# Kernel tuning notes

Hardware: AMD Instinct MI355X
Metric: run time of the kernel (lower is better)

Reference implementation:

```python
import jax, jax.numpy as jnp
import numpy as np
import math

S, B, H, NH = 2048, 2, 2048, 16
HN = H // NH  # 128, head dim


def _rope_cache(seq_len, hn):
    # inv_freqs over even indices, half_hn entries
    inv_freqs = 0.0001 ** (jnp.arange(0, hn, 2, dtype=jnp.float32) / hn)
    pos = jnp.arange(seq_len, dtype=jnp.float32)
    angles = pos[:, None] * inv_freqs  # [s, hn/2]
    return jnp.cos(angles), jnp.sin(angles)


def _apply_rope(x, cos, sin):
    # x: [s, b, np, hn]; cos/sin: [s, hn/2] broadcast over b, np
    half = x.shape[-1] // 2
    c = cos[:, None, None, :]
    s = sin[:, None, None, :]
    left, right = x[..., :half], x[..., half:]
    return jnp.concatenate((c * left - s * right, s * left + c * right), axis=-1)


def setup_inputs() -> dict:
    key = jax.random.key(0)
    k0, k1, k2 = jax.random.split(key, 3)
    hidden_states = jax.random.normal(k0, (S, B, H), dtype=jnp.float32)
    # causal additive mask, broadcast over batch and heads
    causal = jnp.tril(jnp.ones((S, S), dtype=bool))
    attention_mask = jnp.where(causal, 0.0, -1e9).astype(jnp.float32)[None, None]
    W_qkv = jax.random.normal(k1, (3 * H, H), dtype=jnp.float32) * 0.02
    b_qkv = jnp.zeros((3 * H,), dtype=jnp.float32)
    W_dense = jax.random.normal(k2, (H, H), dtype=jnp.float32) * 0.02
    b_dense = jnp.zeros((H,), dtype=jnp.float32)
    return {"hidden_states": hidden_states, "attention_mask": attention_mask,
            "W_qkv": W_qkv, "b_qkv": b_qkv, "W_dense": W_dense, "b_dense": b_dense}


def reference(hidden_states, attention_mask, W_qkv, b_qkv, W_dense, b_dense):
    s, b, h = hidden_states.shape
    # fused QKV projection: [s,b,3h] -> [s,b,np,3*hn] -> split per head
    mixed = hidden_states @ W_qkv.T + b_qkv
    mixed = mixed.reshape(s, b, NH, 3 * HN)
    q, k, v = jnp.split(mixed, 3, axis=-1)  # each [s,b,np,hn]
    cos, sin = _rope_cache(s, HN)
    q = _apply_rope(q, cos, sin)
    k = _apply_rope(k, cos, sin)
    norm_factor = math.sqrt(HN)  # coeff is None (scale_attn_by_inverse_layer_idx=False)
    scores = jnp.einsum('sbnh,tbnh->bnst', q, k) / norm_factor  # [b,np,sq,sk]
    scores = scores + attention_mask
    probs = jax.nn.softmax(scores, axis=-1)  # dropout p=0 in eval
    ctx = jnp.einsum('bnst,tbnh->sbnh', probs, v).reshape(s, b, h)
    return ctx @ W_dense.T + b_dense  # [s,b,h]
```

## Files before the change

### kernel.cpp

```cpp
#include <hip/hip_runtime.h>

#define SEQ   2048
#define BATCH 2
#define HID   2048
#define NHEAD 16
#define HDIM  128
#define MTOT  4096
#define KDIM  2048

typedef __attribute__((ext_vector_type(8))) short  bf16x8;
typedef __attribute__((ext_vector_type(4))) float  f32x4;
typedef __attribute__((ext_vector_type(4))) unsigned short u16x4;
typedef __attribute__((ext_vector_type(8))) unsigned short u16x8;

__device__ __forceinline__ unsigned short f2bf(float x) {
  unsigned u = __float_as_uint(x);
  u += 0x7fffu + ((u >> 16) & 1u);
  return (unsigned short)(u >> 16);
}

__device__ __forceinline__ float fexp2(float x) {
  float r;
  asm("v_exp_f32 %0, %1" : "=v"(r) : "v"(x));
  return r;
}

__device__ __forceinline__ void gl_lds16(const void* g, void* l) {
  __builtin_amdgcn_global_load_lds(
      (__attribute__((address_space(1))) void*)g,
      (__attribute__((address_space(3))) void*)l, 16, 0, 0);
}

__device__ __forceinline__ f32x4 mfma16(bf16x8 a, bf16x8 b, f32x4 c) {
  return __builtin_amdgcn_mfma_f32_16x16x32_bf16(a, b, c, 0, 0, 0);
}

__global__ __launch_bounds__(256, 8)
void conv_swz(const float* __restrict__ src, unsigned short* __restrict__ dst) {
  int i = blockIdx.x * 256 + threadIdx.x;
  int base = i << 2;
  int r = base >> 11, k = base & 2047;
  f32x4 v = *(const f32x4*)(src + base);
  int kp = k ^ (((r >> 1) & 3) << 3);
  u16x4 o;
  o[0] = f2bf(v[0]); o[1] = f2bf(v[1]); o[2] = f2bf(v[2]); o[3] = f2bf(v[3]);
  *(u16x4*)(dst + (size_t)r * 2048 + kp) = o;
}

__global__ __launch_bounds__(256, 8)
void rope_cache_k(float* __restrict__ cosT, float* __restrict__ sinT) {
  int idx = blockIdx.x * 256 + threadIdx.x;
  int s = idx >> 6, i = idx & 63;
  float inv = powf(1e-4f, (float)i * (1.0f / 64.0f));
  float a = (float)s * inv;
  cosT[idx] = cosf(a);
  sinT[idx] = sinf(a);
}

template<int EPI>
__global__ __launch_bounds__(512, 2)
void gemm8p(const unsigned short* __restrict__ A,
            const unsigned short* __restrict__ Bt,
            const float* __restrict__ bias,
            unsigned short* __restrict__ Qs,
            unsigned short* __restrict__ Ks,
            unsigned short* __restrict__ Vp,
            const float* __restrict__ cosT,
            const float* __restrict__ sinT,
            float* __restrict__ Cout)
{
  __shared__ alignas(16) short lds[65536];
  const int tid = threadIdx.x;
  const int wid = tid >> 6, lane = tid & 63, g = lane >> 4, c = lane & 15;
  const int wr = wid >> 1, wc = wid & 1;
  const int m0 = blockIdx.y << 8, n0 = blockIdx.x << 8;

  char* ldsb = (char*)lds;
  const int slotg = (g ^ ((c >> 1) & 3)) << 4;
  const char* ldsAr = ldsb + ((wr * 64 + c) * 64 + slotg);
  const char* ldsBr = ldsb + 65536 + ((wc * 128 + c) * 64 + slotg);

  const char* gA = (const char*)A  + (size_t)(m0 + (tid >> 2)) * 4096 + (tid & 3) * 16;
  const char* gB = (const char*)Bt + (size_t)(n0 + (tid >> 2)) * 4096 + (tid & 3) * 16;
  char* lA = ldsb + tid * 16;
  char* lB = ldsb + 65536 + tid * 16;

#define STG_A(T, KS, BUF) do { int _ko = (T) * 128 + (KS) * 64;            \
    gl_lds16(gA + _ko,          lA + ((BUF) * 2 + (KS)) * 16384);          \
    gl_lds16(gA + _ko + 524288, lA + ((BUF) * 2 + (KS)) * 16384 + 8192); } while (0)
#define STG_B(T, KS, BUF) do { int _ko = (T) * 128 + (KS) * 64;            \
    gl_lds16(gB + _ko,          lB + ((BUF) * 2 + (KS)) * 16384);          \
    gl_lds16(gB + _ko + 524288, lB + ((BUF) * 2 + (KS)) * 16384 + 8192); } while (0)

  f32x4 acc[4][8];
#pragma unroll
  for (int i = 0; i < 4; ++i)
#pragma unroll
    for (int j = 0; j < 8; ++j) {
      acc[i][j][0] = 0.f; acc[i][j][1] = 0.f; acc[i][j][2] = 0.f; acc[i][j][3] = 0.f;
    }

  bf16x8 a[4], b[4];

#define LDA(KS, BUF) do { _Pragma("unroll")                                 \
    for (int mf = 0; mf < 4; ++mf)                                          \
      a[mf] = *(const bf16x8*)(ldsAr + ((BUF) * 2 + (KS)) * 16384 + mf * 1024); } while (0)
#define LDB(KS, NH, BUF) do { _Pragma("unroll")                             \
    for (int nf = 0; nf < 4; ++nf)                                          \
      b[nf] = *(const bf16x8*)(ldsBr + ((BUF) * 2 + (KS)) * 16384 + ((NH) * 4 + nf) * 1024); } while (0)

#define PHASE(NH, KS, BUF, STAGE, VMW) do {                                 \
    if ((NH) == 0) { LDA(KS, BUF); }                                        \
    LDB(KS, NH, BUF);                                                       \
    STAGE;                                                                  \
    __builtin_amdgcn_s_barrier();                                           \
    asm volatile("s_waitcnt lgkmcnt(0)" ::: "memory");                      \
    __builtin_amdgcn_s_setprio(1);                                          \
    _Pragma("unroll")                                                       \
    for (int mf = 0; mf < 4; ++mf)                                          \
      _Pragma("unroll")                                                     \
      for (int nf = 0; nf < 4; ++nf)                                        \
        acc[mf][(NH) * 4 + nf] = mfma16(a[mf], b[nf], acc[mf][(NH) * 4 + nf]); \
    __builtin_amdgcn_s_setprio(0);                                          \
    VMW;                                                                    \
    __builtin_amdgcn_s_barrier();                                           \
  } while (0)

  const int NT = KDIM / 64;

  STG_A(0, 0, 0); STG_B(0, 0, 0); STG_A(0, 1, 0); STG_B(0, 1, 0);
  STG_A(1, 0, 1); STG_B(1, 0, 1); STG_A(1, 1, 1);
  asm volatile("s_waitcnt vmcnt(6)" ::: "memory");
  __builtin_amdgcn_s_barrier();

#define GROUP(T, BUF) do {                                                  \
    PHASE(0, 0, BUF, { if ((T) + 1 < NT) STG_B((T) + 1, 1, (BUF) ^ 1); }, ((void)0)); \
    PHASE(1, 0, BUF, { if ((T) + 2 < NT) STG_A((T) + 2, 0, (BUF)); },  ((void)0));    \
    PHASE(0, 1, BUF, { if ((T) + 2 < NT) STG_B((T) + 2, 0, (BUF)); },  ((void)0));    \
    PHASE(1, 1, BUF, { if ((T) + 2 < NT) STG_A((T) + 2, 1, (BUF)); },               \
      { if ((T) + 2 < NT) { asm volatile("s_waitcnt vmcnt(6)" ::: "memory"); }      \
        else              { asm volatile("s_waitcnt vmcnt(0)" ::: "memory"); } });  \
  } while (0)

  for (int t = 0; t < NT; t += 2) {
    GROUP(t, 0);
    GROUP(t + 1, 1);
  }

  if (EPI == 0) {
    const int pbase = n0 + wc * 128;
    const int nh = pbase / 384;
    const int type = (pbase % 384) >> 7;
    if (type < 2) {
      unsigned short* dst = (type == 0) ? Qs : Ks;
      const float qsc = (type == 0) ? 0.08838834764831845f * 1.4426950408889634f : 1.0f;
#pragma unroll
      for (int mf = 0; mf < 4; ++mf)
#pragma unroll
        for (int rr = 0; rr < 4; ++rr) {
          int m = m0 + wr * 64 + mf * 16 + g * 4 + rr;
          int s = m >> 1, bb = m & 1;
          size_t plane = (size_t)(bb * NHEAD + nh) * (SEQ * HDIM);
          int swb = (s & 7) << 3;
#pragma unroll
          for (int nf = 0; nf < 4; ++nf) {
            int dl = nf * 16 + c;
            float xl = acc[mf][nf][rr]     + bias[pbase + dl];
            float xr = acc[mf][nf + 4][rr] + bias[pbase + 64 + dl];
            float co = cosT[s * 64 + dl], si = sinT[s * 64 + dl];
            dst[plane + (size_t)s * HDIM + (dl ^ swb)]        = f2bf((co * xl - si * xr) * qsc);
            dst[plane + (size_t)s * HDIM + ((dl + 64) ^ swb)] = f2bf((si * xl + co * xr) * qsc);
          }
        }
    } else {
#pragma unroll
      for (int mf = 0; mf < 4; ++mf)
#pragma unroll
        for (int rr = 0; rr < 4; ++rr) {
          int m = m0 + wr * 64 + mf * 16 + g * 4 + rr;
          int s = m >> 1, bb = m & 1;
          size_t plane = (size_t)(bb * NHEAD + nh) * (SEQ * HDIM);
#pragma unroll
          for (int nf = 0; nf < 8; ++nf) {
            int d = nf * 16 + c;
            Vp[plane + (size_t)s * HDIM + d] = f2bf(acc[mf][nf][rr] + bias[pbase + d]);
          }
        }
    }
  } else {
#pragma unroll
    for (int mf = 0; mf < 4; ++mf)
#pragma unroll
      for (int rr = 0; rr < 4; ++rr) {
        int m = m0 + wr * 64 + mf * 16 + g * 4 + rr;
#pragma unroll
        for (int nf = 0; nf < 8; ++nf) {
          int n = n0 + wc * 128 + nf * 16 + c;
          Cout[(size_t)m * HID + n] = acc[mf][nf][rr] + bias[n];
        }
      }
  }
#undef GROUP
#undef PHASE
#undef LDA
#undef LDB
#undef STG_A
#undef STG_B
}

__global__ __launch_bounds__(256, 4)
void transpose_v(const unsigned short* __restrict__ Vp, unsigned short* __restrict__ Vt) {
  __shared__ alignas(16) unsigned short T[64 * 136];
  const int plane = blockIdx.x >> 5;
  const int t0 = (blockIdx.x & 31) << 6;
  const size_t pbase = (size_t)plane * (SEQ * HDIM);
  const int tid = threadIdx.x;
  {
    int t = tid >> 2, d0 = (tid & 3) << 5;
    const unsigned short* src = Vp + pbase + (size_t)(t0 + t) * HDIM + d0;
#pragma unroll
    for (int j = 0; j < 4; ++j) {
      u16x8 v = *(const u16x8*)(src + j * 8);
      *(u16x8*)(&T[t * 136 + d0 + j * 8]) = v;
    }
  }
  __syncthreads();
  {
    int d = tid >> 1, half = tid & 1;
    unsigned short* dstp = Vt + pbase + (size_t)d * SEQ;
    int swb = (d & 7) << 3;
#pragma unroll
    for (int gg = 0; gg < 4; ++gg) {
      u16x8 v;
#pragma unroll
      for (int e = 0; e < 8; ++e)
        v[e] = T[(half * 32 + gg * 8 + e) * 136 + d];
      int tloc = half * 32 + gg * 8;
      *(u16x8*)(dstp + ((t0 + tloc) ^ swb)) = v;
    }
  }
}

__global__ __launch_bounds__(256, 2)
void attn(const unsigned short* __restrict__ Qs,
          const unsigned short* __restrict__ Ks,
          const unsigned short* __restrict__ Vt,
          unsigned short* __restrict__ ctx)
{
  __shared__ alignas(16) unsigned short Klds[2][64 * 128];
  __shared__ alignas(16) unsigned short Vlds[128 * 64];
  __shared__ alignas(16) unsigned short Plds[128 * 72];
  const int tid = threadIdx.x;
  const int w = tid >> 6, lane = tid & 63, g = lane >> 4, c = lane & 15;
  const int bid = blockIdx.x;
  const int head = bid & 31;
  const int qb = (bid < 256) ? (15 - (bid >> 5)) : ((bid >> 5) - 8);
  const int q0 = qb << 7;
  const size_t plane = (size_t)head * (SEQ * HDIM);
  const unsigned short* Qp = Qs + plane;
  const unsigned short* Kp = Ks + plane;
  const unsigned short* Vp = Vt + plane;

  bf16x8 qf[2][4];
#pragma unroll
  for (int q2 = 0; q2 < 2; ++q2) {
    int s = q0 + w * 32 + q2 * 16 + c;
    int swb = (s & 7) << 3;
#pragma unroll
    for (int kk = 0; kk < 4; ++kk) {
      int d0 = kk * 32 + g * 8;
      qf[q2][kk] = *(const bf16x8*)(Qp + (size_t)s * HDIM + (d0 ^ swb));
    }
  }

  f32x4 accO[2][8];
#pragma unroll
  for (int i = 0; i < 2; ++i)
#pragma unroll
    for (int j = 0; j < 8; ++j) {
      accO[i][j][0] = 0.f; accO[i][j][1] = 0.f; accO[i][j][2] = 0.f; accO[i][j][3] = 0.f;
    }
  float mrun[2] = { -1e30f, -1e30f };
  float lrun[2] = { 0.f, 0.f };

  const char* KgBase = (const char*)Kp + (tid >> 4) * 256 + (tid & 15) * 16;
  const char* VgBase = (const char*)Vp + (size_t)(tid >> 3) * 4096 + (tid & 7) * 16;
  char* VldsW = (char*)Vlds + w * 1024;

  const int ntiles = (q0 >> 6) + 2;
  const int qminw = q0 + w * 32;
  const int qmaxw = qminw + 31;

#pragma unroll
  for (int i = 0; i < 4; ++i)
    gl_lds16(KgBase, (char*)Klds[0] + w * 1024 + i * 4096), KgBase += 4096;
  KgBase -= 16384;

  for (int kt = 0; kt < ntiles; ++kt) {
    const int t0 = kt << 6;
    const bool havenext = (kt + 1 < ntiles);

#pragma unroll
    for (int i = 0; i < 4; ++i)
      gl_lds16(VgBase + t0 * 2 + (size_t)i * 131072, VldsW + i * 4096);
    if (havenext) {
      char* kdst = (char*)Klds[(kt + 1) & 1] + w * 1024;
#pragma unroll
      for (int i = 0; i < 4; ++i)
        gl_lds16(KgBase + (size_t)(t0 + 64) * 256 + i * 4096, kdst + i * 4096);
    }
    if (havenext) asm volatile("s_waitcnt vmcnt(8)" ::: "memory");
    else          asm volatile("s_waitcnt vmcnt(4)" ::: "memory");
    __builtin_amdgcn_s_barrier();

    if (t0 <= qmaxw) {
      const char* Kb = (const char*)Klds[kt & 1];
      f32x4 sacc[4][2];
#pragma unroll
      for (int i = 0; i < 4; ++i)
#pragma unroll
        for (int j = 0; j < 2; ++j) {
          sacc[i][j][0] = 0.f; sacc[i][j][1] = 0.f; sacc[i][j][2] = 0.f; sacc[i][j][3] = 0.f;
        }
      __builtin_amdgcn_s_setprio(1);
#pragma unroll
      for (int kk = 0; kk < 4; ++kk) {
        bf16x8 kf[4];
#pragma unroll
        for (int ta = 0; ta < 4; ++ta) {
          int t = ta * 16 + c;
          int d0 = kk * 32 + g * 8;
          kf[ta] = *(const bf16x8*)(Kb + t * 256 + ((d0 ^ ((t & 7) << 3)) << 1));
        }
#pragma unroll
        for (int ta = 0; ta < 4; ++ta)
#pragma unroll
          for (int q2 = 0; q2 < 2; ++q2)
            sacc[ta][q2] = mfma16(kf[ta], qf[q2][kk], sacc[ta][q2]);
      }
      __builtin_amdgcn_s_setprio(0);

      if (t0 + 63 > qminw) {
#pragma unroll
        for (int ta = 0; ta < 4; ++ta)
#pragma unroll
          for (int q2 = 0; q2 < 2; ++q2)
#pragma unroll
            for (int r = 0; r < 4; ++r) {
              int t = t0 + ta * 16 + g * 4 + r;
              int q = qminw + q2 * 16 + c;
              if (t > q) sacc[ta][q2][r] = -30000.f;
            }
      }

      float corr[2];
      bool resc = false;
#pragma unroll
      for (int q2 = 0; q2 < 2; ++q2) {
        float mx = -30000.f;
#pragma unroll
        for (int ta = 0; ta < 4; ++ta)
          mx = fmaxf(mx, fmaxf(fmaxf(sacc[ta][q2][0], sacc[ta][q2][1]),
                               fmaxf(sacc[ta][q2][2], sacc[ta][q2][3])));
        mx = fmaxf(mx, __shfl_xor(mx, 16));
        mx = fmaxf(mx, __shfl_xor(mx, 32));
        bool rs = mx > mrun[q2] + 8.0f;
        resc |= rs;
        float mnew = rs ? mx : mrun[q2];
        corr[q2] = fexp2(mrun[q2] - mnew);
        mrun[q2] = mnew;
        float ls = 0.f;
#pragma unroll
        for (int ta = 0; ta < 4; ++ta)
#pragma unroll
          for (int r = 0; r < 4; ++r) {
            float e = fexp2(sacc[ta][q2][r] - mnew);
            sacc[ta][q2][r] = e;
            ls += e;
          }
        ls += __shfl_xor(ls, 16);
        ls += __shfl_xor(ls, 32);
        lrun[q2] = lrun[q2] * corr[q2] + ls;
      }

      if (__any(resc)) {
#pragma unroll
        for (int q2 = 0; q2 < 2; ++q2)
#pragma unroll
          for (int r = 0; r < 4; ++r) {
            float cD = __shfl(corr[q2], (lane & 48) | (((lane >> 4) << 2) + r));
#pragma unroll
            for (int fn = 0; fn < 8; ++fn) accO[q2][fn][r] *= cD;
          }
      }

#pragma unroll
      for (int q2 = 0; q2 < 2; ++q2) {
        int prow = w * 32 + q2 * 16 + c;
#pragma unroll
        for (int ta = 0; ta < 4; ++ta) {
          u16x4 pk;
          pk[0] = f2bf(sacc[ta][q2][0]); pk[1] = f2bf(sacc[ta][q2][1]);
          pk[2] = f2bf(sacc[ta][q2][2]); pk[3] = f2bf(sacc[ta][q2][3]);
          *(u16x4*)(&Plds[prow * 72 + ta * 16 + g * 4]) = pk;
        }
      }
    }

    if (havenext) asm volatile("s_waitcnt vmcnt(4)" ::: "memory");
    else          asm volatile("s_waitcnt vmcnt(0)" ::: "memory");
    __builtin_amdgcn_s_barrier();

    if (t0 <= qmaxw) {
      __builtin_amdgcn_s_setprio(1);
#pragma unroll
      for (int kk = 0; kk < 2; ++kk) {
        bf16x8 pa[2];
#pragma unroll
        for (int q2 = 0; q2 < 2; ++q2)
          pa[q2] = *(const bf16x8*)((const char*)Plds + (w * 32 + q2 * 16 + c) * 144 + (kk * 32 + g * 8) * 2);
#pragma unroll
        for (int fn = 0; fn < 8; ++fn) {
          int d = fn * 16 + c;
          int tt = kk * 32 + g * 8;
          bf16x8 vb = *(const bf16x8*)((const char*)Vlds + d * 128 + ((tt ^ ((d & 7) << 3)) << 1));
#pragma unroll
          for (int q2 = 0; q2 < 2; ++q2)
            accO[q2][fn] = mfma16(pa[q2], vb, accO[q2][fn]);
        }
      }
      __builtin_amdgcn_s_setprio(0);
    }
    __builtin_amdgcn_s_barrier();
  }

  const int b = head >> 4, nh = head & 15;
  float linv[2] = { 1.0f / lrun[0], 1.0f / lrun[1] };
#pragma unroll
  for (int q2 = 0; q2 < 2; ++q2)
#pragma unroll
    for (int r = 0; r < 4; ++r) {
      float inv = __shfl(linv[q2], (lane & 48) | (((lane >> 4) << 2) + r));
      int q = q0 + w * 32 + q2 * 16 + g * 4 + r;
      int m = q * 2 + b;
      int swb = ((m >> 1) & 3) << 3;
#pragma unroll
      for (int fn = 0; fn < 8; ++fn) {
        int h = nh * 128 + fn * 16 + c;
        ctx[(size_t)m * HID + (h ^ swb)] = f2bf(accO[q2][fn][r] * inv);
      }
    }
}

extern "C" void kernel_launch(void* const* d_in, const int* in_sizes, int n_in,
                              void* d_out, int out_size, void* d_ws, size_t ws_size,
                              hipStream_t stream) {
  const float* hidden = (const float*)d_in[0];
  const float* Wqkv = (const float*)d_in[2];
  const float* bqkv = (const float*)d_in[3];
  const float* Wd   = (const float*)d_in[4];
  const float* bd   = (const float*)d_in[5];
  float* out = (float*)d_out;
  char* ws = (char*)d_ws;

  const size_t OFF_HID  = 0;
  const size_t OFF_WQKV = 16777216;
  const size_t OFF_WD   = 41943040;
  const size_t OFF_COS  = 50331648;
  const size_t OFF_SIN  = 50855936;
  const size_t OFF_Q    = 51380224;
  const size_t OFF_K    = 68157440;
  const size_t OFF_V    = 84934656;
  const size_t OFF_VT   = 101711872;
  if (ws_size < 118489088) return;

  unsigned short* hidb  = (unsigned short*)(ws + OFF_HID);
  unsigned short* wqkvb = (unsigned short*)(ws + OFF_WQKV);
  unsigned short* wdb   = (unsigned short*)(ws + OFF_WD);
  float* cosT = (float*)(ws + OFF_COS);
  float* sinT = (float*)(ws + OFF_SIN);
  unsigned short* Qsb = (unsigned short*)(ws + OFF_Q);
  unsigned short* Ksb = (unsigned short*)(ws + OFF_K);
  unsigned short* Vpb = (unsigned short*)(ws + OFF_V);
  unsigned short* Vtb = (unsigned short*)(ws + OFF_VT);
  unsigned short* ctxb = hidb;

  conv_swz<<<8192, 256, 0, stream>>>(hidden, hidb);
  conv_swz<<<12288, 256, 0, stream>>>(Wqkv, wqkvb);
  conv_swz<<<4096, 256, 0, stream>>>(Wd, wdb);
  rope_cache_k<<<512, 256, 0, stream>>>(cosT, sinT);

  gemm8p<0><<<dim3(24, 16), 512, 0, stream>>>(hidb, wqkvb, bqkv,
                                              Qsb, Ksb, Vpb, cosT, sinT, nullptr);
  transpose_v<<<1024, 256, 0, stream>>>(Vpb, Vtb);
  attn<<<512, 256, 0, stream>>>(Qsb, Ksb, Vtb, ctxb);
  gemm8p<1><<<dim3(8, 16), 512, 0, stream>>>(ctxb, wdb, bd,
                                             nullptr, nullptr, nullptr, nullptr, nullptr, out);
}
```

Baseline: 280.3 us.

## Add dedicated QKV GEMM with per-head 256x384 tiles and triple-buffered LDS

Replaces the generic 256x256-tile QKV GEMM with a dedicated kernel. Each block computes one full head's Q, K and V (256 rows by 384 columns), which gives 256 blocks, one wave on 256 CUs, instead of 384. It uses a three-stage LDS ring (120KB) with a grid swizzle for L2 locality, and a simpler epilogue where each lane handles matching Q/K/V columns and reuses the cos/sin values. This is meant to remove the partial second wave and improve operand reuse, at the cost of large LDS use (one block per CU) and more accumulator registers.

After: 508.1 us. 1.81x slower.

```diff
diff --git a/kernel.cpp b/kernel.cpp
--- a/kernel.cpp
+++ b/kernel.cpp
@@ -57,16 +57,134 @@
   sinT[idx] = sinf(a);
 }
 
+__global__ __launch_bounds__(512, 2)
+void gemm_qkv(const unsigned short* __restrict__ A,
+              const unsigned short* __restrict__ Bt,
+              const float* __restrict__ bias,
+              unsigned short* __restrict__ Qs,
+              unsigned short* __restrict__ Ks,
+              unsigned short* __restrict__ Vp,
+              const float* __restrict__ cosT,
+              const float* __restrict__ sinT)
+{
+  __shared__ alignas(16) char lds[122880];
+  const int tid = threadIdx.x;
+  const int wid = tid >> 6, lane = tid & 63, g = lane >> 4, c = lane & 15;
+  const int wr = wid >> 2, wc = wid & 3;
+
+  const int bid = blockIdx.x;
+  const int swz = (bid & 7) * 32 + (bid >> 3);
+  const int mblk = swz & 15, nblk = swz >> 4;
+  const int m0 = mblk << 8;
+  const int n0 = nblk * 384;
+  const int nh = nblk;
+
+  char* ldsb = (char*)lds;
+  const int slotg = (g ^ ((c >> 1) & 3)) << 4;
+  const char* ldsAr = ldsb + (wr * 128 + c) * 64 + slotg;
+  const char* ldsBr = ldsb + 49152 + (wc * 16 + c) * 64 + slotg;
+
+  const char* gA = (const char*)A  + (size_t)(m0 + (tid >> 2)) * 4096 + (tid & 3) * 16;
+  const char* gB = (const char*)Bt + (size_t)(n0 + (tid >> 2)) * 4096 + (tid & 3) * 16;
+  char* lA = ldsb + tid * 16;
+  char* lB = ldsb + 49152 + tid * 16;
+
+#define STG_A(T, BUF) do { const char* _g = gA + (T) * 64; char* _l = lA + (BUF) * 16384; \
+    gl_lds16(_g, _l); gl_lds16(_g + 524288, _l + 8192); } while (0)
+#define STG_B(T, BUF) do { const char* _g = gB + (T) * 64; char* _l = lB + (BUF) * 24576; \
+    gl_lds16(_g, _l); gl_lds16(_g + 524288, _l + 8192); gl_lds16(_g + 1048576, _l + 16384); } while (0)
+
+  f32x4 acc[8][6];
+#pragma unroll
+  for (int i = 0; i < 8; ++i)
+#pragma unroll
+    for (int j = 0; j < 6; ++j) {
+      acc[i][j][0] = 0.f; acc[i][j][1] = 0.f; acc[i][j][2] = 0.f; acc[i][j][3] = 0.f;
+    }
+
+  bf16x8 a[4], b[6];
+  const int NT = KDIM / 32;
+
+#define PH(T, BUF, MH, STAGE, VMW) do {                                     \
+    _Pragma("unroll")                                                       \
+    for (int mf = 0; mf < 4; ++mf)                                          \
+      a[mf] = *(const bf16x8*)(ldsAr + (BUF) * 16384 + (MH) * 4096 + mf * 1024); \
+    if ((MH) == 0) {                                                        \
+      _Pragma("unroll")                                                     \
+      for (int nl = 0; nl < 6; ++nl)                                        \
+        b[nl] = *(const bf16x8*)(ldsBr + (BUF) * 24576 + nl * 4096);        \
+    }                                                                       \
+    STAGE;                                                                  \
+    __builtin_amdgcn_s_barrier();                                           \
+    asm volatile("s_waitcnt lgkmcnt(0)" ::: "memory");                      \
+    __builtin_amdgcn_s_setprio(1);                                          \
+    _Pragma("unroll")                                                       \
+    for (int mf = 0; mf < 4; ++mf)                                          \
+      _Pragma("unroll")                                                     \
+      for (int nl = 0; nl < 6; ++nl)                                        \
+        acc[(MH) * 4 + mf][nl] = mfma16(a[mf], b[nl], acc[(MH) * 4 + mf][nl]); \
+    __builtin_amdgcn_s_setprio(0);                                          \
+    VMW;                                                                    \
+    __builtin_amdgcn_s_barrier();                                           \
+  } while (0)
+
+#define TILE(T, BUF, BUF2) do {                                             \
+    PH(T, BUF, 0, { if ((T) + 2 < NT) STG_A((T) + 2, BUF2); }, ((void)0));  \
+    PH(T, BUF, 1, { if ((T) + 2 < NT) STG_B((T) + 2, BUF2); },              \
+       { if ((T) + 2 < NT) { asm volatile("s_waitcnt vmcnt(5)" ::: "memory"); } \
+         else              { asm volatile("s_waitcnt vmcnt(0)" ::: "memory"); } }); \
+  } while (0)
+
+  STG_A(0, 0); STG_B(0, 0);
+  STG_A(1, 1); STG_B(1, 1);
+  asm volatile("s_waitcnt vmcnt(5)" ::: "memory");
+  __builtin_amdgcn_s_barrier();
+
+  for (int t = 0; t < 63; t += 3) {
+    TILE(t, 0, 2);
+    TILE(t + 1, 1, 0);
+    TILE(t + 2, 2, 1);
+  }
+  TILE(63, 0, 2);
+
+  const float qsc = 0.08838834764831845f * 1.4426950408889634f;
+  const int dl = wc * 16 + c;
+#pragma unroll
+  for (int ar = 0; ar < 8; ++ar) {
+#pragma unroll
+    for (int rr = 0; rr < 4; ++rr) {
+      int m = m0 + wr * 128 + ar * 16 + g * 4 + rr;
+      int s = m >> 1, bb = m & 1;
+      size_t plane = (size_t)(bb * NHEAD + nh) * (SEQ * HDIM);
+      int swb = (s & 7) << 3;
+      float co = cosT[s * 64 + dl], si = sinT[s * 64 + dl];
+      {
+        float xl = acc[ar][0][rr] + bias[n0 + dl];
+        float xr = acc[ar][1][rr] + bias[n0 + 64 + dl];
+        Qs[plane + (size_t)s * HDIM + (dl ^ swb)]        = f2bf((co * xl - si * xr) * qsc);
+        Qs[plane + (size_t)s * HDIM + ((dl + 64) ^ swb)] = f2bf((si * xl + co * xr) * qsc);
+      }
+      {
+        float xl = acc[ar][2][rr] + bias[n0 + 128 + dl];
+        float xr = acc[ar][3][rr] + bias[n0 + 192 + dl];
+        Ks[plane + (size_t)s * HDIM + (dl ^ swb)]        = f2bf(co * xl - si * xr);
+        Ks[plane + (size_t)s * HDIM + ((dl + 64) ^ swb)] = f2bf(si * xl + co * xr);
+      }
+      Vp[plane + (size_t)s * HDIM + dl]      = f2bf(acc[ar][4][rr] + bias[n0 + 256 + dl]);
+      Vp[plane + (size_t)s * HDIM + dl + 64] = f2bf(acc[ar][5][rr] + bias[n0 + 320 + dl]);
+    }
+  }
+#undef TILE
+#undef PH
+#undef STG_A
+#undef STG_B
+}
+
 template<int EPI>
 __global__ __launch_bounds__(512, 2)
 void gemm8p(const unsigned short* __restrict__ A,
             const unsigned short* __restrict__ Bt,
             const float* __restrict__ bias,
-            unsigned short* __restrict__ Qs,
-            unsigned short* __restrict__ Ks,
-            unsigned short* __restrict__ Vp,
-            const float* __restrict__ cosT,
-            const float* __restrict__ sinT,
             float* __restrict__ Cout)
 {
   __shared__ alignas(16) short lds[65536];
@@ -147,59 +265,17 @@
     GROUP(t + 1, 1);
   }
 
-  if (EPI == 0) {
-    const int pbase = n0 + wc * 128;
-    const int nh = pbase / 384;
-    const int type = (pbase % 384) >> 7;
-    if (type < 2) {
-      unsigned short* dst = (type == 0) ? Qs : Ks;
-      const float qsc = (type == 0) ? 0.08838834764831845f * 1.4426950408889634f : 1.0f;
-#pragma unroll
-      for (int mf = 0; mf < 4; ++mf)
-#pragma unroll
-        for (int rr = 0; rr < 4; ++rr) {
-          int m = m0 + wr * 64 + mf * 16 + g * 4 + rr;
-          int s = m >> 1, bb = m & 1;
-          size_t plane = (size_t)(bb * NHEAD + nh) * (SEQ * HDIM);
-          int swb = (s & 7) << 3;
-#pragma unroll
-          for (int nf = 0; nf < 4; ++nf) {
-            int dl = nf * 16 + c;
-            float xl = acc[mf][nf][rr]     + bias[pbase + dl];
-            float xr = acc[mf][nf + 4][rr] + bias[pbase + 64 + dl];
-            float co = cosT[s * 64 + dl], si = sinT[s * 64 + dl];
-            dst[plane + (size_t)s * HDIM + (dl ^ swb)]        = f2bf((co * xl - si * xr) * qsc);
-            dst[plane + (size_t)s * HDIM + ((dl + 64) ^ swb)] = f2bf((si * xl + co * xr) * qsc);
-          }
-        }
-    } else {
-#pragma unroll
-      for (int mf = 0; mf < 4; ++mf)
-#pragma unroll
-        for (int rr = 0; rr < 4; ++rr) {
-          int m = m0 + wr * 64 + mf * 16 + g * 4 + rr;
-          int s = m >> 1, bb = m & 1;
-          size_t plane = (size_t)(bb * NHEAD + nh) * (SEQ * HDIM);
-#pragma unroll
-          for (int nf = 0; nf < 8; ++nf) {
-            int d = nf * 16 + c;
-            Vp[plane + (size_t)s * HDIM + d] = f2bf(acc[mf][nf][rr] + bias[pbase + d]);
-          }
-        }
-    }
-  } else {
-#pragma unroll
-    for (int mf = 0; mf < 4; ++mf)
-#pragma unroll
-      for (int rr = 0; rr < 4; ++rr) {
-        int m = m0 + wr * 64 + mf * 16 + g * 4 + rr;
-#pragma unroll
-        for (int nf = 0; nf < 8; ++nf) {
-          int n = n0 + wc * 128 + nf * 16 + c;
-          Cout[(size_t)m * HID + n] = acc[mf][nf][rr] + bias[n];
-        }
-      }
-  }
+#pragma unroll
+  for (int mf = 0; mf < 4; ++mf)
+#pragma unroll
+    for (int rr = 0; rr < 4; ++rr) {
+      int m = m0 + wr * 64 + mf * 16 + g * 4 + rr;
+#pragma unroll
+      for (int nf = 0; nf < 8; ++nf) {
+        int n = n0 + wc * 128 + nf * 16 + c;
+        Cout[(size_t)m * HID + n] = acc[mf][nf][rr] + bias[n];
+      }
+    }
 #undef GROUP
 #undef PHASE
 #undef LDA
@@ -490,10 +566,8 @@
   conv_swz<<<4096, 256, 0, stream>>>(Wd, wdb);
   rope_cache_k<<<512, 256, 0, stream>>>(cosT, sinT);
 
-  gemm8p<0><<<dim3(24, 16), 512, 0, stream>>>(hidb, wqkvb, bqkv,
-                                              Qsb, Ksb, Vpb, cosT, sinT, nullptr);
+  gemm_qkv<<<256, 512, 0, stream>>>(hidb, wqkvb, bqkv, Qsb, Ksb, Vpb, cosT, sinT);
   transpose_v<<<1024, 256, 0, stream>>>(Vpb, Vtb);
   attn<<<512, 256, 0, stream>>>(Qsb, Ksb, Vtb, ctxb);
-  gemm8p<1><<<dim3(8, 16), 512, 0, stream>>>(ctxb, wdb, bd,
-                                             nullptr, nullptr, nullptr, nullptr, nullptr, out);
-}
+  gemm8p<1><<<dim3(8, 16), 512, 0, stream>>>(ctxb, wdb, bd, out);
+}
```
